# Kernel optimization log

Hardware: AMD Instinct MI355X
Metric: run time of the kernel (lower is better)

Reference implementation:

```python
import jax, jax.numpy as jnp
import numpy as np
from jax.ops import segment_sum, segment_max

N, E = 50000, 500000
F_IN, H, D1, D2, EDIM, HID = 388, 8, 64, 128, 16, 32


def gatv2(x, edge_index, edge_attr, Wl, Wr, We, att, bias, concat):
    # PyG GATv2Conv with edge_dim, add_self_loops=True, fill_value='mean', eval mode (no dropout)
    n = x.shape[0]
    h, d = att.shape
    src, dst = edge_index[0], edge_index[1]
    deg = segment_sum(jnp.ones(src.shape, x.dtype), dst, num_segments=n)
    loop_attr = segment_sum(edge_attr, dst, num_segments=n) / jnp.maximum(deg, 1.0)[:, None]
    loops = jnp.arange(n)
    src = jnp.concatenate([src, loops])
    dst = jnp.concatenate([dst, loops])
    ea = jnp.concatenate([edge_attr, loop_attr], axis=0)
    xl = (x @ Wl).reshape(n, h, d)   # source transform (lin_l)
    xr = (x @ Wr).reshape(n, h, d)   # target transform (lin_r)
    ee = (ea @ We).reshape(-1, h, d)
    m = jax.nn.leaky_relu(xl[src] + xr[dst] + ee, 0.2)   # [E+N, h, d]
    score = jnp.einsum('ehd,hd->eh', m, att)              # [E+N, h]
    smax = segment_max(score, dst, num_segments=n)        # every node has a self-loop
    alpha = jnp.exp(score - smax[dst])
    denom = segment_sum(alpha, dst, num_segments=n)
    alpha = alpha / denom[dst]
    out = segment_sum(alpha[:, :, None] * xl[src], dst, num_segments=n)  # [n, h, d]
    out = out.reshape(n, h * d) if concat else out.mean(axis=1)
    return out + bias


def setup_inputs():
    key = jax.random.key(0)
    ks = jax.random.split(key, 24)
    p = lambda k, shape: (jax.random.normal(k, shape, jnp.float32) * 0.05)
    return {
        'x': jax.random.normal(ks[0], (N, F_IN), jnp.float32),
        'edge_index': jax.random.randint(ks[1], (2, E), 0, N),
        'edge_attr': jax.random.normal(ks[2], (E, EDIM), jnp.float32),
        'Wl1': p(ks[3], (F_IN, H * D1)), 'Wr1': p(ks[4], (F_IN, H * D1)),
        'We1': p(ks[5], (EDIM, H * D1)), 'att1': p(ks[6], (H, D1)), 'b1': p(ks[7], (H * D1,)),
        'Wl2': p(ks[8], (H * D1, H * D2)), 'Wr2': p(ks[9], (H * D1, H * D2)),
        'We2': p(ks[10], (EDIM, H * D2)), 'att2': p(ks[11], (H, D2)), 'b2': p(ks[12], (D2,)),
        'W_ih': p(ks[13], (4 * HID, D2)), 'W_hh': p(ks[14], (4 * HID, HID)),
        'b_ih': p(ks[15], (4 * HID,)), 'b_hh': p(ks[16], (4 * HID,)),
        'fcW': p(ks[17], (1, HID)), 'fcb': p(ks[18], (1,)),
    }


def reference(x, edge_index, edge_attr, Wl1, Wr1, We1, att1, b1,
              Wl2, Wr2, We2, att2, b2, W_ih, W_hh, b_ih, b_hh, fcW, fcb):
    h = jnp.tanh(gatv2(x, edge_index, edge_attr, Wl1, Wr1, We1, att1, b1, True))
    h = jnp.tanh(gatv2(h, edge_index, edge_attr, Wl2, Wr2, We2, att2, b2, False))
    # single-step LSTM, h0=c0=0; W_hh @ h0 == 0 but biases remain
    gates = h @ W_ih.T + b_ih + b_hh                      # [N, 4*HID]
    i, f, g, o = jnp.split(gates, 4, axis=1)
    c = jax.nn.sigmoid(i) * jnp.tanh(g)
    hidden = jax.nn.sigmoid(o) * jnp.tanh(c)              # [N, HID]
    return hidden @ fcW.T + fcb                           # [N, 1]
```

## Files before the change

kernel.cpp:

```cpp
#include <hip/hip_runtime.h>

#define N_NODES 50000
#define N_EDGES 500000
#define F_INDIM 388
#define H_HEADS 8
#define DD1 64
#define DD2 128
#define EDIM 16
#define HIDN 32

#define M_PAD 50048
#define K1_PAD 416

typedef unsigned short u16;
typedef unsigned int u32;
typedef __attribute__((ext_vector_type(8))) short bf16x8;
typedef __attribute__((ext_vector_type(4))) float f32x4;

static __device__ __forceinline__ float bfu2f(u32 lo16) {
  union { u32 u; float f; } c;
  c.u = lo16 << 16;
  return c.f;
}
static __device__ __forceinline__ u16 f2bf(float f) {
  union { float f; u32 u; } c;
  c.f = f;
  u32 u = c.u + 0x7fffu + ((c.u >> 16) & 1u);
  return (u16)(u >> 16);
}

static __device__ __forceinline__ float waveSum(float v) {
#pragma unroll
  for (int off = 32; off > 0; off >>= 1) v += __shfl_xor(v, off, 64);
  return v;
}
static __device__ __forceinline__ void waveSum4(float& a, float& b, float& c, float& d) {
#pragma unroll
  for (int off = 32; off > 0; off >>= 1) {
    a += __shfl_xor(a, off, 64);
    b += __shfl_xor(b, off, 64);
    c += __shfl_xor(c, off, 64);
    d += __shfl_xor(d, off, 64);
  }
}

static __device__ __forceinline__ void gl_lds16(const void* g, void* l) {
  __builtin_amdgcn_global_load_lds((const __attribute__((address_space(1))) u32*)g,
                                   (__attribute__((address_space(3))) u32*)l, 16, 0, 0);
}

__global__ void k_zero(float* __restrict__ out, int n) {
  int i = blockIdx.x * blockDim.x + threadIdx.x;
  if (i < n) out[i] = 0.f;
}

__global__ void k_hist(const int* __restrict__ dst, int* __restrict__ deg) {
  int e = blockIdx.x * blockDim.x + threadIdx.x;
  if (e < N_EDGES) atomicAdd(&deg[dst[e]], 1);
}

__global__ __launch_bounds__(1024) void k_scan(const int* __restrict__ deg,
                                               int* __restrict__ row_start) {
  __shared__ int wsum[16];
  __shared__ int carry_s;
  int tid = threadIdx.x;
  int lane = tid & 63, wv = tid >> 6;
  if (tid == 0) carry_s = 0;
  __syncthreads();
  for (int base = 0; base < N_NODES; base += 1024) {
    int i = base + tid;
    int v = (i < N_NODES) ? deg[i] : 0;
    int inc = v;
#pragma unroll
    for (int off = 1; off < 64; off <<= 1) {
      int t = __shfl_up(inc, off, 64);
      if (lane >= off) inc += t;
    }
    if (lane == 63) wsum[wv] = inc;
    __syncthreads();
    if (wv == 0 && lane < 16) {
      int s = wsum[lane];
#pragma unroll
      for (int off = 1; off < 16; off <<= 1) {
        int t = __shfl_up(s, off, 64);
        if (lane >= off) s += t;
      }
      wsum[lane] = s;
    }
    __syncthreads();
    int add = (wv > 0) ? wsum[wv - 1] : 0;
    int ex = carry_s + add + inc - v;
    if (i < N_NODES) row_start[i] = ex;
    __syncthreads();
    if (tid == 0) carry_s += wsum[15];
    __syncthreads();
  }
  if (threadIdx.x == 0) row_start[N_NODES] = carry_s;
}

__global__ void k_scatter(const int* __restrict__ dst, const int* __restrict__ src,
                          const int* __restrict__ row_start, int* __restrict__ cursor,
                          int* __restrict__ eid, int* __restrict__ srcp) {
  int e = blockIdx.x * blockDim.x + threadIdx.x;
  if (e < N_EDGES) {
    int d = dst[e];
    int pos = row_start[d] + atomicAdd(&cursor[d], 1);
    eid[pos] = e;
    srcp[pos] = src[e];
  }
}

__global__ __launch_bounds__(256) void k_la(const float* __restrict__ ea,
                                            const int* __restrict__ eid,
                                            const int* __restrict__ row_start,
                                            float* __restrict__ la) {
  int node = blockIdx.x * 16 + (threadIdx.x >> 4);
  int k = threadIdx.x & 15;
  if (node >= N_NODES) return;
  int r0 = row_start[node], r1 = row_start[node + 1];
  float s = 0.f;
  for (int i = r0; i < r1; ++i) s += ea[(size_t)eid[i] * EDIM + k];
  la[node * EDIM + k] = s / (float)max(r1 - r0, 1);
}

__global__ void k_cvt_x(const float* __restrict__ x, u16* __restrict__ xb) {
  long t = (long)blockIdx.x * 256 + threadIdx.x;
  if (t >= (long)M_PAD * K1_PAD) return;
  int row = (int)(t / K1_PAD);
  int col = (int)(t % K1_PAD);
  float v = (row < N_NODES && col < F_INDIM) ? x[(size_t)row * F_INDIM + col] : 0.f;
  xb[t] = f2bf(v);
}

__global__ void k_cvt_wT(const float* __restrict__ W, u16* __restrict__ WT, int K, int N, int Kp) {
  int t = blockIdx.x * 256 + threadIdx.x;
  if (t >= N * Kp) return;
  int n = t / Kp, k = t % Kp;
  WT[t] = f2bf(k < K ? W[(size_t)k * N + n] : 0.f);
}

__global__ void k_cvt(const float* __restrict__ W, u16* __restrict__ O, int n) {
  int t = blockIdx.x * 256 + threadIdx.x;
  if (t < n) O[t] = f2bf(W[t]);
}

template <bool CF32>
__global__ __launch_bounds__(256) void gemm_mfma(const u16* __restrict__ A,
                                                 const u16* __restrict__ BT,
                                                 void* __restrict__ Cv, int M, int Nd, int K,
                                                 int lda, int ldb) {
  __shared__ u16 As[128 * 32];
  __shared__ u16 Bs[128 * 32];
  int tid = threadIdx.x;
  int lane = tid & 63;
  int wv = tid >> 6;
  int m_base = blockIdx.y * 128;
  int n_base = blockIdx.x * 128;
  int wrow = (wv >> 1) * 64;
  int wcol = (wv & 1) * 64;
  f32x4 acc[4][4];
#pragma unroll
  for (int i = 0; i < 4; ++i)
#pragma unroll
    for (int j = 0; j < 4; ++j)
#pragma unroll
      for (int r = 0; r < 4; ++r) acc[i][j][r] = 0.f;

  for (int k0 = 0; k0 < K; k0 += 32) {
    __syncthreads();
#pragma unroll
    for (int it = 0; it < 2; ++it) {
      int t = it * 256 + tid;
      int row = t >> 2;
      int kc = (t & 3) * 8;
      gl_lds16(A + (size_t)(m_base + row) * lda + k0 + kc, As + (size_t)(it * 256 + wv * 64) * 8);
      gl_lds16(BT + (size_t)(n_base + row) * ldb + k0 + kc, Bs + (size_t)(it * 256 + wv * 64) * 8);
    }
    __syncthreads();
    bf16x8 af[4], bfr[4];
#pragma unroll
    for (int i = 0; i < 4; ++i) {
      int r = wrow + i * 16 + (lane & 15);
      af[i] = *(const bf16x8*)(As + r * 32 + (lane >> 4) * 8);
    }
#pragma unroll
    for (int j = 0; j < 4; ++j) {
      int r = wcol + j * 16 + (lane & 15);
      bfr[j] = *(const bf16x8*)(Bs + r * 32 + (lane >> 4) * 8);
    }
#pragma unroll
    for (int i = 0; i < 4; ++i)
#pragma unroll
      for (int j = 0; j < 4; ++j)
        acc[i][j] = __builtin_amdgcn_mfma_f32_16x16x32_bf16(af[i], bfr[j], acc[i][j], 0, 0, 0);
  }
#pragma unroll
  for (int i = 0; i < 4; ++i) {
    int grow_base = m_base + wrow + i * 16 + (lane >> 4) * 4;
#pragma unroll
    for (int j = 0; j < 4; ++j) {
      int gcol = n_base + wcol + j * 16 + (lane & 15);
#pragma unroll
      for (int r = 0; r < 4; ++r) {
        int grow = grow_base + r;
        if (grow < M) {
          float v = acc[i][j][r];
          if (CF32)
            ((float*)Cv)[(size_t)grow * Nd + gcol] = v;
          else
            ((u16*)Cv)[(size_t)grow * Nd + gcol] = f2bf(v);
        }
      }
    }
  }
}

__global__ __launch_bounds__(512) void k_gat1(
    const u16* __restrict__ xlr, const float* __restrict__ ea, const float* __restrict__ We,
    const float* __restrict__ att, const float* __restrict__ bias, const int* __restrict__ srcp,
    const int* __restrict__ eid, const int* __restrict__ row_start, const float* __restrict__ la,
    u16* __restrict__ out) {
  int n = blockIdx.x;
  int col = threadIdx.x;
  int r0 = row_start[n], r1 = row_start[n + 1];
  float Wc[EDIM];
#pragma unroll
  for (int k = 0; k < EDIM; ++k) Wc[k] = We[k * 512 + col];
  float a = att[col];
  float attA = 0.6f * a, attB = 0.4f * a;
  float xrd = bfu2f(xlr[(size_t)n * 1024 + 512 + col]);
  float xlself = bfu2f(xlr[(size_t)n * 1024 + col]);

  auto escore = [&](int e, float xv) -> float {
    const float4* ea4 = (const float4*)(ea + (size_t)e * EDIM);
    float4 v0 = ea4[0], v1 = ea4[1], v2 = ea4[2], v3 = ea4[3];
    float t = v0.x * Wc[0];
    t = fmaf(v0.y, Wc[1], t);
    t = fmaf(v0.z, Wc[2], t);
    t = fmaf(v0.w, Wc[3], t);
    t = fmaf(v1.x, Wc[4], t);
    t = fmaf(v1.y, Wc[5], t);
    t = fmaf(v1.z, Wc[6], t);
    t = fmaf(v1.w, Wc[7], t);
    t = fmaf(v2.x, Wc[8], t);
    t = fmaf(v2.y, Wc[9], t);
    t = fmaf(v2.z, Wc[10], t);
    t = fmaf(v2.w, Wc[11], t);
    t = fmaf(v3.x, Wc[12], t);
    t = fmaf(v3.y, Wc[13], t);
    t = fmaf(v3.z, Wc[14], t);
    t = fmaf(v3.w, Wc[15], t);
    float z = xv + xrd + t;
    return fmaf(attA, z, attB * fabsf(z));
  };

  float acc = 0.f, denom = 0.f;
  int i = r0;
  for (; i + 4 <= r1; i += 4) {
    int e0 = eid[i], e1 = eid[i + 1], e2 = eid[i + 2], e3 = eid[i + 3];
    int s0 = srcp[i], s1 = srcp[i + 1], s2 = srcp[i + 2], s3 = srcp[i + 3];
    float x0 = bfu2f(xlr[(size_t)s0 * 1024 + col]);
    float x1 = bfu2f(xlr[(size_t)s1 * 1024 + col]);
    float x2 = bfu2f(xlr[(size_t)s2 * 1024 + col]);
    float x3 = bfu2f(xlr[(size_t)s3 * 1024 + col]);
    float p0 = escore(e0, x0);
    float p1 = escore(e1, x1);
    float p2 = escore(e2, x2);
    float p3 = escore(e3, x3);
    waveSum4(p0, p1, p2, p3);
    float w0 = __expf(p0), w1 = __expf(p1), w2 = __expf(p2), w3 = __expf(p3);
    acc = fmaf(w0, x0, acc);
    acc = fmaf(w1, x1, acc);
    acc = fmaf(w2, x2, acc);
    acc = fmaf(w3, x3, acc);
    denom += (w0 + w1) + (w2 + w3);
  }
  for (; i < r1; ++i) {
    int e = eid[i], s = srcp[i];
    float xv = bfu2f(xlr[(size_t)s * 1024 + col]);
    float p = waveSum(escore(e, xv));
    float w = __expf(p);
    acc = fmaf(w, xv, acc);
    denom += w;
  }
  float ee = 0.f;
#pragma unroll
  for (int k = 0; k < EDIM; ++k) ee = fmaf(la[n * EDIM + k], Wc[k], ee);
  float z = xlself + xrd + ee;
  float sc = waveSum(fmaf(attA, z, attB * fabsf(z)));
  float w = __expf(sc);
  acc = fmaf(w, xlself, acc);
  denom += w;
  out[(size_t)n * 512 + col] = f2bf(tanhf(acc / denom + bias[col]));
}

__global__ __launch_bounds__(512) void k_gat2(
    const u16* __restrict__ xlr, const float* __restrict__ ea, const float* __restrict__ We,
    const float* __restrict__ att, const float* __restrict__ bias, const int* __restrict__ srcp,
    const int* __restrict__ eid, const int* __restrict__ row_start, const float* __restrict__ la,
    u16* __restrict__ out) {
  int n = blockIdx.x;
  int tid = threadIdx.x;
  int lane = tid & 63;
  int h = tid >> 6;
  __shared__ float hsum[H_HEADS][DD2];
  int r0 = row_start[n], r1 = row_start[n + 1];
  int col = h * DD2 + lane * 2;
  float Wcx[EDIM], Wcy[EDIM];
#pragma unroll
  for (int k = 0; k < EDIM; ++k) {
    float2 t = *(const float2*)(We + k * 1024 + col);
    Wcx[k] = t.x;
    Wcy[k] = t.y;
  }
  float2 av = *(const float2*)(att + col);
  float attAx = 0.6f * av.x, attBx = 0.4f * av.x;
  float attAy = 0.6f * av.y, attBy = 0.4f * av.y;
  u32 xru = *(const u32*)(xlr + (size_t)n * 2048 + 1024 + col);
  u32 xlu = *(const u32*)(xlr + (size_t)n * 2048 + col);
  float xrdx = bfu2f(xru & 0xffff), xrdy = bfu2f(xru >> 16);
  float xlsx = bfu2f(xlu & 0xffff), xlsy = bfu2f(xlu >> 16);

  auto escore2 = [&](int e, float xvx, float xvy) -> float {
    const float4* ea4 = (const float4*)(ea + (size_t)e * EDIM);
    float4 v0 = ea4[0], v1 = ea4[1], v2 = ea4[2], v3 = ea4[3];
    float ex = v0.x * Wcx[0], ey = v0.x * Wcy[0];
    ex = fmaf(v0.y, Wcx[1], ex); ey = fmaf(v0.y, Wcy[1], ey);
    ex = fmaf(v0.z, Wcx[2], ex); ey = fmaf(v0.z, Wcy[2], ey);
    ex = fmaf(v0.w, Wcx[3], ex); ey = fmaf(v0.w, Wcy[3], ey);
    ex = fmaf(v1.x, Wcx[4], ex); ey = fmaf(v1.x, Wcy[4], ey);
    ex = fmaf(v1.y, Wcx[5], ex); ey = fmaf(v1.y, Wcy[5], ey);
    ex = fmaf(v1.z, Wcx[6], ex); ey = fmaf(v1.z, Wcy[6], ey);
    ex = fmaf(v1.w, Wcx[7], ex); ey = fmaf(v1.w, Wcy[7], ey);
    ex = fmaf(v2.x, Wcx[8], ex); ey = fmaf(v2.x, Wcy[8], ey);
    ex = fmaf(v2.y, Wcx[9], ex); ey = fmaf(v2.y, Wcy[9], ey);
    ex = fmaf(v2.z, Wcx[10], ex); ey = fmaf(v2.z, Wcy[10], ey);
    ex = fmaf(v2.w, Wcx[11], ex); ey = fmaf(v2.w, Wcy[11], ey);
    ex = fmaf(v3.x, Wcx[12], ex); ey = fmaf(v3.x, Wcy[12], ey);
    ex = fmaf(v3.y, Wcx[13], ex); ey = fmaf(v3.y, Wcy[13], ey);
    ex = fmaf(v3.z, Wcx[14], ex); ey = fmaf(v3.z, Wcy[14], ey);
    ex = fmaf(v3.w, Wcx[15], ex); ey = fmaf(v3.w, Wcy[15], ey);
    float zx = xvx + xrdx + ex, zy = xvy + xrdy + ey;
    float p = fmaf(attAx, zx, attBx * fabsf(zx));
    p = fmaf(attAy, zy, p);
    p = fmaf(attBy, fabsf(zy), p);
    return p;
  };

  float accx = 0.f, accy = 0.f, denom = 0.f;
  int i = r0;
  for (; i + 4 <= r1; i += 4) {
    int e0 = eid[i], e1 = eid[i + 1], e2 = eid[i + 2], e3 = eid[i + 3];
    int s0 = srcp[i], s1 = srcp[i + 1], s2 = srcp[i + 2], s3 = srcp[i + 3];
    u32 u0 = *(const u32*)(xlr + (size_t)s0 * 2048 + col);
    u32 u1 = *(const u32*)(xlr + (size_t)s1 * 2048 + col);
    u32 u2 = *(const u32*)(xlr + (size_t)s2 * 2048 + col);
    u32 u3 = *(const u32*)(xlr + (size_t)s3 * 2048 + col);
    float x0x = bfu2f(u0 & 0xffff), x0y = bfu2f(u0 >> 16);
    float x1x = bfu2f(u1 & 0xffff), x1y = bfu2f(u1 >> 16);
    float x2x = bfu2f(u2 & 0xffff), x2y = bfu2f(u2 >> 16);
    float x3x = bfu2f(u3 & 0xffff), x3y = bfu2f(u3 >> 16);
    float p0 = escore2(e0, x0x, x0y);
    float p1 = escore2(e1, x1x, x1y);
    float p2 = escore2(e2, x2x, x2y);
    float p3 = escore2(e3, x3x, x3y);
    waveSum4(p0, p1, p2, p3);
    float w0 = __expf(p0), w1 = __expf(p1), w2 = __expf(p2), w3 = __expf(p3);
    accx = fmaf(w0, x0x, accx); accy = fmaf(w0, x0y, accy);
    accx = fmaf(w1, x1x, accx); accy = fmaf(w1, x1y, accy);
    accx = fmaf(w2, x2x, accx); accy = fmaf(w2, x2y, accy);
    accx = fmaf(w3, x3x, accx); accy = fmaf(w3, x3y, accy);
    denom += (w0 + w1) + (w2 + w3);
  }
  for (; i < r1; ++i) {
    int e = eid[i], s = srcp[i];
    u32 u0 = *(const u32*)(xlr + (size_t)s * 2048 + col);
    float xvx = bfu2f(u0 & 0xffff), xvy = bfu2f(u0 >> 16);
    float p = waveSum(escore2(e, xvx, xvy));
    float w = __expf(p);
    accx = fmaf(w, xvx, accx);
    accy = fmaf(w, xvy, accy);
    denom += w;
  }
  float eex = 0.f, eey = 0.f;
#pragma unroll
  for (int k = 0; k < EDIM; ++k) {
    float lv = la[n * EDIM + k];
    eex = fmaf(lv, Wcx[k], eex);
    eey = fmaf(lv, Wcy[k], eey);
  }
  float zx = xlsx + xrdx + eex, zy = xlsy + xrdy + eey;
  float ps = fmaf(attAx, zx, attBx * fabsf(zx));
  ps = fmaf(attAy, zy, ps);
  ps = fmaf(attBy, fabsf(zy), ps);
  float sc = waveSum(ps);
  float w = __expf(sc);
  accx = fmaf(w, xlsx, accx);
  accy = fmaf(w, xlsy, accy);
  denom += w;

  float inv = 1.f / denom;
  hsum[h][lane * 2] = accx * inv;
  hsum[h][lane * 2 + 1] = accy * inv;
  __syncthreads();
  if (tid < DD2) {
    float s = 0.f;
#pragma unroll
    for (int hh = 0; hh < H_HEADS; ++hh) s += hsum[hh][tid];
    out[(size_t)n * DD2 + tid] = f2bf(tanhf(s * 0.125f + bias[tid]));
  }
}

__global__ __launch_bounds__(128) void k_lstm(const float* __restrict__ gates,
                                              const float* __restrict__ b_ih,
                                              const float* __restrict__ b_hh,
                                              const float* __restrict__ fcW,
                                              const float* __restrict__ fcb,
                                              float* __restrict__ out) {
  int n = blockIdx.x;
  int j = threadIdx.x;
  __shared__ float gs[128];
  gs[j] = gates[(size_t)n * 128 + j] + b_ih[j] + b_hh[j];
  __syncthreads();
  if (j < 32) {
    float iv = gs[j], gv = gs[64 + j], ov = gs[96 + j];
    float c = (1.f / (1.f + __expf(-iv))) * tanhf(gv);
    float hd = (1.f / (1.f + __expf(-ov))) * tanhf(c);
    float p = hd * fcW[j];
#pragma unroll
    for (int off = 16; off > 0; off >>= 1) p += __shfl_down(p, off, 32);
    if (j == 0) out[n] = p + fcb[0];
  }
}

extern "C" void kernel_launch(void* const* d_in, const int* in_sizes, int n_in, void* d_out,
                              int out_size, void* d_ws, size_t ws_size, hipStream_t stream) {
  const float* x = (const float*)d_in[0];
  const int* ei = (const int*)d_in[1];
  const float* ea = (const float*)d_in[2];
  const float* Wl1 = (const float*)d_in[3];
  const float* Wr1 = (const float*)d_in[4];
  const float* We1 = (const float*)d_in[5];
  const float* att1 = (const float*)d_in[6];
  const float* b1 = (const float*)d_in[7];
  const float* Wl2 = (const float*)d_in[8];
  const float* Wr2 = (const float*)d_in[9];
  const float* We2 = (const float*)d_in[10];
  const float* att2 = (const float*)d_in[11];
  const float* b2 = (const float*)d_in[12];
  const float* W_ih = (const float*)d_in[13];
  const float* b_ih = (const float*)d_in[15];
  const float* b_hh = (const float*)d_in[16];
  const float* fcW = (const float*)d_in[17];
  const float* fcb = (const float*)d_in[18];
  float* out = (float*)d_out;
  const int* srcA = ei;
  const int* dstA = ei + N_EDGES;

  char* ws = (char*)d_ws;
  const size_t OFF_XBF = (size_t)N_NODES * 1024 * 2;
  const size_t OFF_H1 = (size_t)N_NODES * 2048 * 2;
  const size_t OFF_GATES = OFF_H1 + (size_t)M_PAD * 128 * 2;
  size_t off = OFF_H1 + (size_t)M_PAD * 512 * 2;
  auto take = [&](size_t bytes) -> char* {
    off = (off + 255) & ~(size_t)255;
    char* p = ws + off;
    off += bytes;
    return p;
  };
  u16* W1T = (u16*)take((size_t)1024 * K1_PAD * 2);
  u16* W2T = (u16*)take((size_t)2048 * 512 * 2);
  u16* WihB = (u16*)take((size_t)128 * 128 * 2);
  int* deg = (int*)take((size_t)N_NODES * 4);
  int* cursor = (int*)take((size_t)N_NODES * 4);
  int* row_start = (int*)take((size_t)(N_NODES + 1) * 4);
  int* eid = (int*)take((size_t)N_EDGES * 4);
  int* srcp = (int*)take((size_t)N_EDGES * 4);
  float* la = (float*)take((size_t)N_NODES * EDIM * 4);

  if (off > ws_size) {
    k_zero<<<(out_size + 255) / 256, 256, 0, stream>>>(out, out_size);
    return;
  }

  u16* xlr1 = (u16*)ws;
  u16* xbf = (u16*)(ws + OFF_XBF);
  u16* xlr2 = (u16*)ws;
  u16* h1 = (u16*)(ws + OFF_H1);
  u16* h2 = (u16*)(ws + OFF_H1);
  float* gates = (float*)(ws + OFF_GATES);

  hipMemsetAsync(deg, 0, (size_t)N_NODES * 4, stream);
  hipMemsetAsync(cursor, 0, (size_t)N_NODES * 4, stream);
  k_hist<<<(N_EDGES + 255) / 256, 256, 0, stream>>>(dstA, deg);
  k_scan<<<1, 1024, 0, stream>>>(deg, row_start);
  k_scatter<<<(N_EDGES + 255) / 256, 256, 0, stream>>>(dstA, srcA, row_start, cursor, eid, srcp);
  k_la<<<(N_NODES + 15) / 16, 256, 0, stream>>>(ea, eid, row_start, la);

  {
    long tot = (long)M_PAD * K1_PAD;
    k_cvt_x<<<(unsigned)((tot + 255) / 256), 256, 0, stream>>>(x, xbf);
    k_cvt_wT<<<(512 * K1_PAD + 255) / 256, 256, 0, stream>>>(Wl1, W1T, F_INDIM, 512, K1_PAD);
    k_cvt_wT<<<(512 * K1_PAD + 255) / 256, 256, 0, stream>>>(Wr1, W1T + (size_t)512 * K1_PAD,
                                                             F_INDIM, 512, K1_PAD);
    k_cvt_wT<<<(1024 * 512 + 255) / 256, 256, 0, stream>>>(Wl2, W2T, 512, 1024, 512);
    k_cvt_wT<<<(1024 * 512 + 255) / 256, 256, 0, stream>>>(Wr2, W2T + (size_t)1024 * 512, 512,
                                                           1024, 512);
    k_cvt<<<(128 * 128 + 255) / 256, 256, 0, stream>>>(W_ih, WihB, 128 * 128);
  }

  const int MB = M_PAD / 128;
  gemm_mfma<false><<<dim3(1024 / 128, MB), 256, 0, stream>>>(xbf, W1T, xlr1, N_NODES, 1024,
                                                             K1_PAD, K1_PAD, K1_PAD);
  k_gat1<<<N_NODES, 512, 0, stream>>>(xlr1, ea, We1, att1, b1, srcp, eid, row_start, la, h1);

  gemm_mfma<false><<<dim3(2048 / 128, MB), 256, 0, stream>>>(h1, W2T, xlr2, N_NODES, 2048, 512,
                                                             512, 512);
  k_gat2<<<N_NODES, 512, 0, stream>>>(xlr2, ea, We2, att2, b2, srcp, eid, row_start, la, h2);

  gemm_mfma<true><<<dim3(1, MB), 256, 0, stream>>>(h2, WihB, gates, N_NODES, 128, 128, 128, 128);
  k_lstm<<<N_NODES, 128, 0, stream>>>(gates, b_ih, b_hh, fcW, fcb, out);
}
```

Measured before the change: 1.535 ms.

## Halve GAT block size with two-wide per-thread columns and packed f32x2 math

Both GAT aggregation kernels now run 256 threads per node instead of 512. Each thread handles 2 columns (layer 1) or 4 columns (layer 2), using f32x2 vector arithmetic so the compiler can emit packed FMA instructions. Each head now spans half a wave, so the score reduction uses a 32-lane shuffle. Edge and source indices are made wave-uniform with readfirstlane, and the scalar remainder loop becomes clamped indices with masked weights. The aim is to cut instruction count, shuffle cost and per-edge redundant edge-attr loads, at the cost of more registers per thread and some wasted work on the padded tail edges.

```diff
diff --git a/kernel.cpp b/kernel.cpp
--- a/kernel.cpp
+++ b/kernel.cpp
@@ -16,32 +16,43 @@
 typedef unsigned int u32;
 typedef __attribute__((ext_vector_type(8))) short bf16x8;
 typedef __attribute__((ext_vector_type(4))) float f32x4;
-
-static __device__ __forceinline__ float bfu2f(u32 lo16) {
-  union { u32 u; float f; } c;
-  c.u = lo16 << 16;
-  return c.f;
-}
+typedef __attribute__((ext_vector_type(2))) float f32x2;
+
 static __device__ __forceinline__ u16 f2bf(float f) {
   union { float f; u32 u; } c;
   c.f = f;
   u32 u = c.u + 0x7fffu + ((c.u >> 16) & 1u);
   return (u16)(u >> 16);
 }
-
-static __device__ __forceinline__ float waveSum(float v) {
-#pragma unroll
-  for (int off = 32; off > 0; off >>= 1) v += __shfl_xor(v, off, 64);
-  return v;
-}
-static __device__ __forceinline__ void waveSum4(float& a, float& b, float& c, float& d) {
-#pragma unroll
-  for (int off = 32; off > 0; off >>= 1) {
+static __device__ __forceinline__ f32x2 bf2f2(u32 u) {
+  union { u32 u; float f; } lo, hi;
+  lo.u = u << 16;
+  hi.u = u & 0xffff0000u;
+  f32x2 r;
+  r.x = lo.f;
+  r.y = hi.f;
+  return r;
+}
+static __device__ __forceinline__ f32x2 abs2(f32x2 v) {
+  f32x2 r;
+  r.x = fabsf(v.x);
+  r.y = fabsf(v.y);
+  return r;
+}
+
+static __device__ __forceinline__ void halfSum4(float& a, float& b, float& c, float& d) {
+#pragma unroll
+  for (int off = 1; off < 32; off <<= 1) {
     a += __shfl_xor(a, off, 64);
     b += __shfl_xor(b, off, 64);
     c += __shfl_xor(c, off, 64);
     d += __shfl_xor(d, off, 64);
   }
+}
+static __device__ __forceinline__ float halfSum(float v) {
+#pragma unroll
+  for (int off = 1; off < 32; off <<= 1) v += __shfl_xor(v, off, 64);
+  return v;
 }
 
 static __device__ __forceinline__ void gl_lds16(const void* g, void* l) {
@@ -215,86 +226,95 @@
   }
 }
 
-__global__ __launch_bounds__(512) void k_gat1(
+__global__ __launch_bounds__(256) void k_gat1(
     const u16* __restrict__ xlr, const float* __restrict__ ea, const float* __restrict__ We,
     const float* __restrict__ att, const float* __restrict__ bias, const int* __restrict__ srcp,
     const int* __restrict__ eid, const int* __restrict__ row_start, const float* __restrict__ la,
     u16* __restrict__ out) {
   int n = blockIdx.x;
-  int col = threadIdx.x;
+  int tid = threadIdx.x;
+  int col = tid * 2;
   int r0 = row_start[n], r1 = row_start[n + 1];
-  float Wc[EDIM];
-#pragma unroll
-  for (int k = 0; k < EDIM; ++k) Wc[k] = We[k * 512 + col];
-  float a = att[col];
-  float attA = 0.6f * a, attB = 0.4f * a;
-  float xrd = bfu2f(xlr[(size_t)n * 1024 + 512 + col]);
-  float xlself = bfu2f(xlr[(size_t)n * 1024 + col]);
-
-  auto escore = [&](int e, float xv) -> float {
+  f32x2 Wc[EDIM];
+#pragma unroll
+  for (int k = 0; k < EDIM; ++k) Wc[k] = *(const f32x2*)(We + k * 512 + col);
+  f32x2 av = *(const f32x2*)(att + col);
+  f32x2 attA = 0.6f * av, attB = 0.4f * av;
+  f32x2 xrd = bf2f2(*(const u32*)(xlr + (size_t)n * 1024 + 512 + col));
+  f32x2 xls = bf2f2(*(const u32*)(xlr + (size_t)n * 1024 + col));
+
+  auto escore = [&](int e, f32x2 xv) -> float {
     const float4* ea4 = (const float4*)(ea + (size_t)e * EDIM);
     float4 v0 = ea4[0], v1 = ea4[1], v2 = ea4[2], v3 = ea4[3];
-    float t = v0.x * Wc[0];
-    t = fmaf(v0.y, Wc[1], t);
-    t = fmaf(v0.z, Wc[2], t);
-    t = fmaf(v0.w, Wc[3], t);
-    t = fmaf(v1.x, Wc[4], t);
-    t = fmaf(v1.y, Wc[5], t);
-    t = fmaf(v1.z, Wc[6], t);
-    t = fmaf(v1.w, Wc[7], t);
-    t = fmaf(v2.x, Wc[8], t);
-    t = fmaf(v2.y, Wc[9], t);
-    t = fmaf(v2.z, Wc[10], t);
-    t = fmaf(v2.w, Wc[11], t);
-    t = fmaf(v3.x, Wc[12], t);
-    t = fmaf(v3.y, Wc[13], t);
-    t = fmaf(v3.z, Wc[14], t);
-    t = fmaf(v3.w, Wc[15], t);
-    float z = xv + xrd + t;
-    return fmaf(attA, z, attB * fabsf(z));
+    f32x2 t = v0.x * Wc[0];
+    t = v0.y * Wc[1] + t;
+    t = v0.z * Wc[2] + t;
+    t = v0.w * Wc[3] + t;
+    t = v1.x * Wc[4] + t;
+    t = v1.y * Wc[5] + t;
+    t = v1.z * Wc[6] + t;
+    t = v1.w * Wc[7] + t;
+    t = v2.x * Wc[8] + t;
+    t = v2.y * Wc[9] + t;
+    t = v2.z * Wc[10] + t;
+    t = v2.w * Wc[11] + t;
+    t = v3.x * Wc[12] + t;
+    t = v3.y * Wc[13] + t;
+    t = v3.z * Wc[14] + t;
+    t = v3.w * Wc[15] + t;
+    f32x2 z = xv + xrd + t;
+    f32x2 q = attA * z + attB * abs2(z);
+    return q.x + q.y;
   };
 
-  float acc = 0.f, denom = 0.f;
-  int i = r0;
-  for (; i + 4 <= r1; i += 4) {
-    int e0 = eid[i], e1 = eid[i + 1], e2 = eid[i + 2], e3 = eid[i + 3];
-    int s0 = srcp[i], s1 = srcp[i + 1], s2 = srcp[i + 2], s3 = srcp[i + 3];
-    float x0 = bfu2f(xlr[(size_t)s0 * 1024 + col]);
-    float x1 = bfu2f(xlr[(size_t)s1 * 1024 + col]);
-    float x2 = bfu2f(xlr[(size_t)s2 * 1024 + col]);
-    float x3 = bfu2f(xlr[(size_t)s3 * 1024 + col]);
+  f32x2 acc = {0.f, 0.f};
+  float denom = 0.f;
+  for (int i = r0; i < r1; i += 4) {
+    int i1 = min(i + 1, r1 - 1), i2 = min(i + 2, r1 - 1), i3 = min(i + 3, r1 - 1);
+    int e0 = __builtin_amdgcn_readfirstlane(eid[i]);
+    int e1 = __builtin_amdgcn_readfirstlane(eid[i1]);
+    int e2 = __builtin_amdgcn_readfirstlane(eid[i2]);
+    int e3 = __builtin_amdgcn_readfirstlane(eid[i3]);
+    int s0 = __builtin_amdgcn_readfirstlane(srcp[i]);
+    int s1 = __builtin_amdgcn_readfirstlane(srcp[i1]);
+    int s2 = __builtin_amdgcn_readfirstlane(srcp[i2]);
+    int s3 = __builtin_amdgcn_readfirstlane(srcp[i3]);
+    f32x2 x0 = bf2f2(*(const u32*)(xlr + (size_t)s0 * 1024 + col));
+    f32x2 x1 = bf2f2(*(const u32*)(xlr + (size_t)s1 * 1024 + col));
+    f32x2 x2 = bf2f2(*(const u32*)(xlr + (size_t)s2 * 1024 + col));
+    f32x2 x3 = bf2f2(*(const u32*)(xlr + (size_t)s3 * 1024 + col));
     float p0 = escore(e0, x0);
     float p1 = escore(e1, x1);
     float p2 = escore(e2, x2);
     float p3 = escore(e3, x3);
-    waveSum4(p0, p1, p2, p3);
+    halfSum4(p0, p1, p2, p3);
     float w0 = __expf(p0), w1 = __expf(p1), w2 = __expf(p2), w3 = __expf(p3);
-    acc = fmaf(w0, x0, acc);
-    acc = fmaf(w1, x1, acc);
-    acc = fmaf(w2, x2, acc);
-    acc = fmaf(w3, x3, acc);
+    if (i + 1 >= r1) w1 = 0.f;
+    if (i + 2 >= r1) w2 = 0.f;
+    if (i + 3 >= r1) w3 = 0.f;
+    acc = w0 * x0 + acc;
+    acc = w1 * x1 + acc;
+    acc = w2 * x2 + acc;
+    acc = w3 * x3 + acc;
     denom += (w0 + w1) + (w2 + w3);
   }
-  for (; i < r1; ++i) {
-    int e = eid[i], s = srcp[i];
-    float xv = bfu2f(xlr[(size_t)s * 1024 + col]);
-    float p = waveSum(escore(e, xv));
-    float w = __expf(p);
-    acc = fmaf(w, xv, acc);
-    denom += w;
-  }
-  float ee = 0.f;
-#pragma unroll
-  for (int k = 0; k < EDIM; ++k) ee = fmaf(la[n * EDIM + k], Wc[k], ee);
-  float z = xlself + xrd + ee;
-  float sc = waveSum(fmaf(attA, z, attB * fabsf(z)));
+  f32x2 ee = {0.f, 0.f};
+#pragma unroll
+  for (int k = 0; k < EDIM; ++k) ee = la[n * EDIM + k] * Wc[k] + ee;
+  f32x2 z = xls + xrd + ee;
+  f32x2 q = attA * z + attB * abs2(z);
+  float sc = halfSum(q.x + q.y);
   float w = __expf(sc);
-  acc = fmaf(w, xlself, acc);
+  acc = w * xls + acc;
   denom += w;
-  out[(size_t)n * 512 + col] = f2bf(tanhf(acc / denom + bias[col]));
-}
-
-__global__ __launch_bounds__(512) void k_gat2(
+  float inv = 1.f / denom;
+  float t0 = tanhf(acc.x * inv + bias[col]);
+  float t1 = tanhf(acc.y * inv + bias[col + 1]);
+  u32 pack = (u32)f2bf(t0) | ((u32)f2bf(t1) << 16);
+  *(u32*)(out + (size_t)n * 512 + col) = pack;
+}
+
+__global__ __launch_bounds__(256) void k_gat2(
     const u16* __restrict__ xlr, const float* __restrict__ ea, const float* __restrict__ We,
     const float* __restrict__ att, const float* __restrict__ bias, const int* __restrict__ srcp,
     const int* __restrict__ eid, const int* __restrict__ row_start, const float* __restrict__ la,
@@ -302,106 +322,111 @@
   int n = blockIdx.x;
   int tid = threadIdx.x;
   int lane = tid & 63;
-  int h = tid >> 6;
+  int wv = tid >> 6;
+  int head = 2 * wv + (lane >> 5);
+  int cih = (lane & 31) * 4;
+  int col = tid * 4;
   __shared__ float hsum[H_HEADS][DD2];
   int r0 = row_start[n], r1 = row_start[n + 1];
-  int col = h * DD2 + lane * 2;
-  float Wcx[EDIM], Wcy[EDIM];
+  f32x2 Wa[EDIM], Wb[EDIM];
 #pragma unroll
   for (int k = 0; k < EDIM; ++k) {
-    float2 t = *(const float2*)(We + k * 1024 + col);
-    Wcx[k] = t.x;
-    Wcy[k] = t.y;
-  }
-  float2 av = *(const float2*)(att + col);
-  float attAx = 0.6f * av.x, attBx = 0.4f * av.x;
-  float attAy = 0.6f * av.y, attBy = 0.4f * av.y;
-  u32 xru = *(const u32*)(xlr + (size_t)n * 2048 + 1024 + col);
-  u32 xlu = *(const u32*)(xlr + (size_t)n * 2048 + col);
-  float xrdx = bfu2f(xru & 0xffff), xrdy = bfu2f(xru >> 16);
-  float xlsx = bfu2f(xlu & 0xffff), xlsy = bfu2f(xlu >> 16);
-
-  auto escore2 = [&](int e, float xvx, float xvy) -> float {
+    float4 t = *(const float4*)(We + k * 1024 + col);
+    Wa[k].x = t.x;
+    Wa[k].y = t.y;
+    Wb[k].x = t.z;
+    Wb[k].y = t.w;
+  }
+  float4 av4 = *(const float4*)(att + col);
+  f32x2 attAa = {0.6f * av4.x, 0.6f * av4.y}, attBa = {0.4f * av4.x, 0.4f * av4.y};
+  f32x2 attAb = {0.6f * av4.z, 0.6f * av4.w}, attBb = {0.4f * av4.z, 0.4f * av4.w};
+  uint2 xru = *(const uint2*)(xlr + (size_t)n * 2048 + 1024 + col);
+  uint2 xlu = *(const uint2*)(xlr + (size_t)n * 2048 + col);
+  f32x2 xrda = bf2f2(xru.x), xrdb = bf2f2(xru.y);
+  f32x2 xlsa = bf2f2(xlu.x), xlsb = bf2f2(xlu.y);
+
+  auto escore = [&](int e, f32x2 xa, f32x2 xb) -> float {
     const float4* ea4 = (const float4*)(ea + (size_t)e * EDIM);
     float4 v0 = ea4[0], v1 = ea4[1], v2 = ea4[2], v3 = ea4[3];
-    float ex = v0.x * Wcx[0], ey = v0.x * Wcy[0];
-    ex = fmaf(v0.y, Wcx[1], ex); ey = fmaf(v0.y, Wcy[1], ey);
-    ex = fmaf(v0.z, Wcx[2], ex); ey = fmaf(v0.z, Wcy[2], ey);
-    ex = fmaf(v0.w, Wcx[3], ex); ey = fmaf(v0.w, Wcy[3], ey);
-    ex = fmaf(v1.x, Wcx[4], ex); ey = fmaf(v1.x, Wcy[4], ey);
-    ex = fmaf(v1.y, Wcx[5], ex); ey = fmaf(v1.y, Wcy[5], ey);
-    ex = fmaf(v1.z, Wcx[6], ex); ey = fmaf(v1.z, Wcy[6], ey);
-    ex = fmaf(v1.w, Wcx[7], ex); ey = fmaf(v1.w, Wcy[7], ey);
-    ex = fmaf(v2.x, Wcx[8], ex); ey = fmaf(v2.x, Wcy[8], ey);
-    ex = fmaf(v2.y, Wcx[9], ex); ey = fmaf(v2.y, Wcy[9], ey);
-    ex = fmaf(v2.z, Wcx[10], ex); ey = fmaf(v2.z, Wcy[10], ey);
-    ex = fmaf(v2.w, Wcx[11], ex); ey = fmaf(v2.w, Wcy[11], ey);
-    ex = fmaf(v3.x, Wcx[12], ex); ey = fmaf(v3.x, Wcy[12], ey);
-    ex = fmaf(v3.y, Wcx[13], ex); ey = fmaf(v3.y, Wcy[13], ey);
-    ex = fmaf(v3.z, Wcx[14], ex); ey = fmaf(v3.z, Wcy[14], ey);
-    ex = fmaf(v3.w, Wcx[15], ex); ey = fmaf(v3.w, Wcy[15], ey);
-    float zx = xvx + xrdx + ex, zy = xvy + xrdy + ey;
-    float p = fmaf(attAx, zx, attBx * fabsf(zx));
-    p = fmaf(attAy, zy, p);
-    p = fmaf(attBy, fabsf(zy), p);
-    return p;
+    f32x2 ta = v0.x * Wa[0], tb = v0.x * Wb[0];
+    ta = v0.y * Wa[1] + ta; tb = v0.y * Wb[1] + tb;
+    ta = v0.z * Wa[2] + ta; tb = v0.z * Wb[2] + tb;
+    ta = v0.w * Wa[3] + ta; tb = v0.w * Wb[3] + tb;
+    ta = v1.x * Wa[4] + ta; tb = v1.x * Wb[4] + tb;
+    ta = v1.y * Wa[5] + ta; tb = v1.y * Wb[5] + tb;
+    ta = v1.z * Wa[6] + ta; tb = v1.z * Wb[6] + tb;
+    ta = v1.w * Wa[7] + ta; tb = v1.w * Wb[7] + tb;
+    ta = v2.x * Wa[8] + ta; tb = v2.x * Wb[8] + tb;
+    ta = v2.y * Wa[9] + ta; tb = v2.y * Wb[9] + tb;
+    ta = v2.z * Wa[10] + ta; tb = v2.z * Wb[10] + tb;
+    ta = v2.w * Wa[11] + ta; tb = v2.w * Wb[11] + tb;
+    ta = v3.x * Wa[12] + ta; tb = v3.x * Wb[12] + tb;
+    ta = v3.y * Wa[13] + ta; tb = v3.y * Wb[13] + tb;
+    ta = v3.z * Wa[14] + ta; tb = v3.z * Wb[14] + tb;
+    ta = v3.w * Wa[15] + ta; tb = v3.w * Wb[15] + tb;
+    f32x2 za = xa + xrda + ta;
+    f32x2 zb = xb + xrdb + tb;
+    f32x2 q = attAa * za + attBa * abs2(za);
+    q = attAb * zb + q;
+    q = attBb * abs2(zb) + q;
+    return q.x + q.y;
   };
 
-  float accx = 0.f, accy = 0.f, denom = 0.f;
-  int i = r0;
-  for (; i + 4 <= r1; i += 4) {
-    int e0 = eid[i], e1 = eid[i + 1], e2 = eid[i + 2], e3 = eid[i + 3];
-    int s0 = srcp[i], s1 = srcp[i + 1], s2 = srcp[i + 2], s3 = srcp[i + 3];
-    u32 u0 = *(const u32*)(xlr + (size_t)s0 * 2048 + col);
-    u32 u1 = *(const u32*)(xlr + (size_t)s1 * 2048 + col);
-    u32 u2 = *(const u32*)(xlr + (size_t)s2 * 2048 + col);
-    u32 u3 = *(const u32*)(xlr + (size_t)s3 * 2048 + col);
-    float x0x = bfu2f(u0 & 0xffff), x0y = bfu2f(u0 >> 16);
-    float x1x = bfu2f(u1 & 0xffff), x1y = bfu2f(u1 >> 16);
-    float x2x = bfu2f(u2 & 0xffff), x2y = bfu2f(u2 >> 16);
-    float x3x = bfu2f(u3 & 0xffff), x3y = bfu2f(u3 >> 16);
-    float p0 = escore2(e0, x0x, x0y);
-    float p1 = escore2(e1, x1x, x1y);
-    float p2 = escore2(e2, x2x, x2y);
-    float p3 = escore2(e3, x3x, x3y);
-    waveSum4(p0, p1, p2, p3);
+  f32x2 acca = {0.f, 0.f}, accb = {0.f, 0.f};
+  float denom = 0.f;
+  for (int i = r0; i < r1; i += 4) {
+    int i1 = min(i + 1, r1 - 1), i2 = min(i + 2, r1 - 1), i3 = min(i + 3, r1 - 1);
+    int e0 = __builtin_amdgcn_readfirstlane(eid[i]);
+    int e1 = __builtin_amdgcn_readfirstlane(eid[i1]);
+    int e2 = __builtin_amdgcn_readfirstlane(eid[i2]);
+    int e3 = __builtin_amdgcn_readfirstlane(eid[i3]);
+    int s0 = __builtin_amdgcn_readfirstlane(srcp[i]);
+    int s1 = __builtin_amdgcn_readfirstlane(srcp[i1]);
+    int s2 = __builtin_amdgcn_readfirstlane(srcp[i2]);
+    int s3 = __builtin_amdgcn_readfirstlane(srcp[i3]);
+    uint2 u0 = *(const uint2*)(xlr + (size_t)s0 * 2048 + col);
+    uint2 u1 = *(const uint2*)(xlr + (size_t)s1 * 2048 + col);
+    uint2 u2 = *(const uint2*)(xlr + (size_t)s2 * 2048 + col);
+    uint2 u3 = *(const uint2*)(xlr + (size_t)s3 * 2048 + col);
+    f32x2 x0a = bf2f2(u0.x), x0b = bf2f2(u0.y);
+    f32x2 x1a = bf2f2(u1.x), x1b = bf2f2(u1.y);
+    f32x2 x2a = bf2f2(u2.x), x2b = bf2f2(u2.y);
+    f32x2 x3a = bf2f2(u3.x), x3b = bf2f2(u3.y);
+    float p0 = escore(e0, x0a, x0b);
+    float p1 = escore(e1, x1a, x1b);
+    float p2 = escore(e2, x2a, x2b);
+    float p3 = escore(e3, x3a, x3b);
+    halfSum4(p0, p1, p2, p3);
     float w0 = __expf(p0), w1 = __expf(p1), w2 = __expf(p2), w3 = __expf(p3);
-    accx = fmaf(w0, x0x, accx); accy = fmaf(w0, x0y, accy);
-    accx = fmaf(w1, x1x, accx); accy = fmaf(w1, x1y, accy);
-    accx = fmaf(w2, x2x, accx); accy = fmaf(w2, x2y, accy);
-    accx = fmaf(w3, x3x, accx); accy = fmaf(w3, x3y, accy);
+    if (i + 1 >= r1) w1 = 0.f;
+    if (i + 2 >= r1) w2 = 0.f;
+    if (i + 3 >= r1) w3 = 0.f;
+    acca = w0 * x0a + acca; accb = w0 * x0b + accb;
+    acca = w1 * x1a + acca; accb = w1 * x1b + accb;
+    acca = w2 * x2a + acca; accb = w2 * x2b + accb;
+    acca = w3 * x3a + acca; accb = w3 * x3b + accb;
     denom += (w0 + w1) + (w2 + w3);
   }
-  for (; i < r1; ++i) {
-    int e = eid[i], s = srcp[i];
-    u32 u0 = *(const u32*)(xlr + (size_t)s * 2048 + col);
-    float xvx = bfu2f(u0 & 0xffff), xvy = bfu2f(u0 >> 16);
-    float p = waveSum(escore2(e, xvx, xvy));
-    float w = __expf(p);
-    accx = fmaf(w, xvx, accx);
-    accy = fmaf(w, xvy, accy);
-    denom += w;
-  }
-  float eex = 0.f, eey = 0.f;
+  f32x2 eea = {0.f, 0.f}, eeb = {0.f, 0.f};
 #pragma unroll
   for (int k = 0; k < EDIM; ++k) {
     float lv = la[n * EDIM + k];
-    eex = fmaf(lv, Wcx[k], eex);
-    eey = fmaf(lv, Wcy[k], eey);
-  }
-  float zx = xlsx + xrdx + eex, zy = xlsy + xrdy + eey;
-  float ps = fmaf(attAx, zx, attBx * fabsf(zx));
-  ps = fmaf(attAy, zy, ps);
-  ps = fmaf(attBy, fabsf(zy), ps);
-  float sc = waveSum(ps);
+    eea = lv * Wa[k] + eea;
+    eeb = lv * Wb[k] + eeb;
+  }
+  f32x2 za = xlsa + xrda + eea, zb = xlsb + xrdb + eeb;
+  f32x2 q = attAa * za + attBa * abs2(za);
+  q = attAb * zb + q;
+  q = attBb * abs2(zb) + q;
+  float sc = halfSum(q.x + q.y);
   float w = __expf(sc);
-  accx = fmaf(w, xlsx, accx);
-  accy = fmaf(w, xlsy, accy);
+  acca = w * xlsa + acca;
+  accb = w * xlsb + accb;
   denom += w;
 
   float inv = 1.f / denom;
-  hsum[h][lane * 2] = accx * inv;
-  hsum[h][lane * 2 + 1] = accy * inv;
+  *(f32x2*)&hsum[head][cih] = acca * inv;
+  *(f32x2*)&hsum[head][cih + 2] = accb * inv;
   __syncthreads();
   if (tid < DD2) {
     float s = 0.f;
@@ -512,11 +537,11 @@
   const int MB = M_PAD / 128;
   gemm_mfma<false><<<dim3(1024 / 128, MB), 256, 0, stream>>>(xbf, W1T, xlr1, N_NODES, 1024,
                                                              K1_PAD, K1_PAD, K1_PAD);
-  k_gat1<<<N_NODES, 512, 0, stream>>>(xlr1, ea, We1, att1, b1, srcp, eid, row_start, la, h1);
+  k_gat1<<<N_NODES, 256, 0, stream>>>(xlr1, ea, We1, att1, b1, srcp, eid, row_start, la, h1);
 
   gemm_mfma<false><<<dim3(2048 / 128, MB), 256, 0, stream>>>(h1, W2T, xlr2, N_NODES, 2048, 512,
                                                              512, 512);
-  k_gat2<<<N_NODES, 512, 0, stream>>>(xlr2, ea, We2, att2, b2, srcp, eid, row_start, la, h2);
+  k_gat2<<<N_NODES, 256, 0, stream>>>(xlr2, ea, We2, att2, b2, srcp, eid, row_start, la, h2);
 
   gemm_mfma<true><<<dim3(1, MB), 256, 0, stream>>>(h2, WihB, gates, N_NODES, 128, 128, 128, 128);
   k_lstm<<<N_NODES, 128, 0, stream>>>(gates, b_ih, b_hh, fcW, fcb, out);
```

Result: faster. 1.370 ms (-10.7%).
